# Optimization experiments

Measured on AMD Instinct MI355X. Metric: run time of the kernel, lower is better.

The kernel has to match this reference:

```python
import jax, jax.numpy as jnp
import numpy as np

# Constants matching init_kwargs
N_HEADS = 8
D_MODEL = 256
PATCH_NUM = 128
D_K = D_MODEL // N_HEADS  # 32
TEMP = 0.5
EPS = 1e-10


def setup_inputs() -> dict:
    key = jax.random.key(0)
    ks = jax.random.split(key, 20)
    s = 0.02
    d, h, n = D_MODEL, N_HEADS, PATCH_NUM
    inp = {
        "x": jax.random.normal(ks[0], (32, n, d), dtype=jnp.float32),
        "gumbel_u": jax.random.uniform(ks[1], (h, n, n, 2), dtype=jnp.float32),
        "memory_w": jax.random.normal(ks[2], (n, h * d), dtype=jnp.float32) * s,
        "fc_out_w": jax.random.normal(ks[3], (2 * d, d), dtype=jnp.float32) * s,
        "fc_out_b": jnp.zeros((d,), jnp.float32),
        "fc_cat_w": jax.random.normal(ks[4], (d, 2), dtype=jnp.float32) * s,
        "fc_cat_b": jnp.zeros((2,), jnp.float32),
        "wq": jax.random.normal(ks[5], (d, d), dtype=jnp.float32) * s,
        "bq": jnp.zeros((d,), jnp.float32),
        "wk": jax.random.normal(ks[6], (d, d), dtype=jnp.float32) * s,
        "bk": jnp.zeros((d,), jnp.float32),
        "wv": jax.random.normal(ks[7], (d, d), dtype=jnp.float32) * s,
        "bv": jnp.zeros((d,), jnp.float32),
        "out_w": jax.random.normal(ks[8], (d, d), dtype=jnp.float32) * s,
        "out_b": jnp.zeros((d,), jnp.float32),
        "mlp_w1": jax.random.normal(ks[9], (d, d), dtype=jnp.float32) * s,
        "mlp_b1": jnp.zeros((d,), jnp.float32),
        "mlp_w2": jax.random.normal(ks[10], (d, d), dtype=jnp.float32) * s,
        "mlp_b2": jnp.zeros((d,), jnp.float32),
    }
    return inp


def _forward(x, memory_w, fc_out_w, fc_out_b, fc_cat_w, fc_cat_b,
             wq, bq, wk, bk, wv, bv, out_w, out_b,
             mlp_w1, mlp_b1, mlp_w2, mlp_b2, gumbel_u):
    H, N, D = N_HEADS, PATCH_NUM, D_MODEL
    B = x.shape[0]

    # ---- SSConnectionLearning on memory feats ----
    # memory: Embedding(N, d_model*n_heads) -> feats [H, N, D]
    feats = memory_w.reshape(N, H, D).transpose(1, 0, 2)
    # rel_rec gathers row index i (receiver), rel_send gathers col index j (sender)
    senders = jnp.broadcast_to(feats[:, None, :, :], (H, N, N, D))   # feats[j]
    receivers = jnp.broadcast_to(feats[:, :, None, :], (H, N, N, D))  # feats[i]
    pair = jnp.concatenate([senders, receivers], axis=-1)  # [H,N,N,2D]
    hdn = jax.nn.relu(jnp.einsum('hijc,cd->hijd', pair, fc_out_w) + fc_out_b)
    logits = jnp.einsum('hijd,dk->hijk', hdn, fc_cat_w) + fc_cat_b  # [H,N,N,2]

    # gumbel-softmax, hard=True, straight-through
    g = -jnp.log(-jnp.log(gumbel_u + EPS) + EPS)
    y_soft = jax.nn.softmax((logits + g) / TEMP, axis=-1)
    y_hard = jax.nn.one_hot(jnp.argmax(y_soft, axis=-1), 2, dtype=y_soft.dtype)
    y = jax.lax.stop_gradient(y_hard - y_soft) + y_soft
    conn = y[..., 1]  # [H,N,N] learned sparse connection mask

    # ---- PatchIntegration (GELU MLP, dropout = identity in eval) ----
    xm = jax.nn.gelu(x @ mlp_w1 + mlp_b1)
    xm = xm @ mlp_w2 + mlp_b2

    # ---- Multihead attention masked by connection matrix ----
    q = (xm @ wq + bq).reshape(B, N, H, D_K).transpose(0, 2, 1, 3)  # [B,H,N,dk]
    k = (xm @ wk + bk).reshape(B, N, H, D_K).transpose(0, 2, 1, 3)
    v = (xm @ wv + bv).reshape(B, N, H, D_K).transpose(0, 2, 1, 3)
    scale = D_K ** -0.5
    scores = jnp.einsum('bhqd,bhkd->bhqk', q, k) * scale
    # additive mask: blocked where conn==0 (large negative keeps softmax finite)
    scores = scores + (conn[None] - 1.0) * 1e9
    attn = jax.nn.softmax(scores, axis=-1)
    out = jnp.einsum('bhqk,bhkd->bhqd', attn, v)
    out = out.transpose(0, 2, 1, 3).reshape(B, N, H * D_K)
    out = out @ out_w + out_b
    return out


def reference(x, gumbel_u, memory_w, fc_out_w, fc_out_b, fc_cat_w, fc_cat_b,
              wq, bq, wk, bk, wv, bv, out_w, out_b,
              mlp_w1, mlp_b1, mlp_w2, mlp_b2):
    return _forward(x, memory_w, fc_out_w, fc_out_b, fc_cat_w, fc_cat_b,
                    wq, bq, wk, bk, wv, bv, out_w, out_b,
                    mlp_w1, mlp_b1, mlp_w2, mlp_b2, gumbel_u)
```

## Files before the change

### kernel.cpp

```cpp
#include <hip/hip_runtime.h>
#include <hip/hip_bf16.h>
#include <math.h>


typedef short short8 __attribute__((ext_vector_type(8)));
typedef float f32x4 __attribute__((ext_vector_type(4)));

union V8 { uint4 u; short8 s; };

__device__ __forceinline__ float gelu_f(float x) {
    float inner = 0.7978845608028654f * (x + 0.044715f * x * x * x);
    return 0.5f * x * (1.0f + tanhf(inner));
}
__device__ __forceinline__ void split_bf16(float x, ushort& h, ushort& l) {
    __hip_bfloat16 bh = __float2bfloat16(x);
    float hf = __bfloat162float(bh);
    __hip_bfloat16 bl = __float2bfloat16(x - hf);
    h = __builtin_bit_cast(ushort, bh);
    l = __builtin_bit_cast(ushort, bl);
}
__device__ __forceinline__ ushort bf16bits(float x) {
    return __builtin_bit_cast(ushort, __float2bfloat16(x));
}
__device__ __forceinline__ float bits_to_f(ushort v) {
    return __builtin_bit_cast(float, ((uint)v) << 16);
}
__device__ __forceinline__ short8 lds_frag(const ushort* p) {
    V8 v; v.u = *(const uint4*)p; return v.s;
}


__global__ __launch_bounds__(512) void k_wprep(
    const float* __restrict__ mlp_w1, const float* __restrict__ mlp_w2,
    const float* __restrict__ wq, const float* __restrict__ wk,
    const float* __restrict__ wv, const float* __restrict__ out_w,
    const float* __restrict__ fc_out_w,
    ushort* __restrict__ hi, ushort* __restrict__ lo) {
    __shared__ __align__(16) float xs2[2][32 * 132];
    int bx = blockIdx.x, t = threadIdx.x;
    int half = t >> 8, tl = t & 255;
    int job = bx * 2 + half;
    int m = job >> 4, ks = (job >> 1) & 7, nh = job & 1;
    const float* W = m == 0 ? mlp_w1 : m == 1 ? mlp_w2 : m == 2 ? wq :
                     m == 3 ? wk : m == 4 ? wv : m == 5 ? out_w :
                     m == 6 ? fc_out_w : fc_out_w + 65536;
    ushort* Hm = hi + m * 65536;
    ushort* Lm = lo + m * 65536;
    float* xs = xs2[half];
    #pragma unroll
    for (int p = 0; p < 4; ++p) {
        int idx = p * 256 + tl;
        int row = idx >> 5, c4 = (idx & 31) * 4;
        *(float4*)(xs + row * 132 + c4) =
            *(const float4*)(W + (ks * 32 + row) * 256 + nh * 128 + c4);
    }
    __syncthreads();
    int lane = tl & 63, lr = lane & 15, quad = lane >> 4;
    #pragma unroll
    for (int it = 0; it < 2; ++it) {
        int tgl = (tl >> 6) + 4 * it;
        int tg = nh * 8 + tgl;
        int nl = tgl * 16 + lr;
        ushort hb[8], lb[8];
        #pragma unroll
        for (int j = 0; j < 8; ++j)
            split_bf16(xs[(quad * 8 + j) * 132 + nl], hb[j], lb[j]);
        uint4 ph = { (uint)hb[0] | ((uint)hb[1] << 16), (uint)hb[2] | ((uint)hb[3] << 16),
                     (uint)hb[4] | ((uint)hb[5] << 16), (uint)hb[6] | ((uint)hb[7] << 16) };
        uint4 pl = { (uint)lb[0] | ((uint)lb[1] << 16), (uint)lb[2] | ((uint)lb[3] << 16),
                     (uint)lb[4] | ((uint)lb[5] << 16), (uint)lb[6] | ((uint)lb[7] << 16) };
        int idx = ((tg * 8 + ks) * 64 + lane) * 8;
        *(uint4*)(Hm + idx) = ph;
        *(uint4*)(Lm + idx) = pl;
    }
}

__global__ __launch_bounds__(512) void k_p2(
    const float* __restrict__ memory_w, const float* __restrict__ X,
    const ushort* __restrict__ Whi, const ushort* __restrict__ Wlo,
    const float* __restrict__ b1, const float* __restrict__ b2,
    const float* __restrict__ Bq, const float* __restrict__ Bk,
    const float* __restrict__ Bv,
    float* __restrict__ A, float* __restrict__ Bm,
    ushort* __restrict__ Q, ushort* __restrict__ K, ushort* __restrict__ V) {
    __shared__ __align__(16) union {
        struct { ushort xhi[16 * 264], xlo[16 * 264]; } f;
        struct {
            ushort aHi[16 * 264], aLo[16 * 264];
            ushort bHi[16 * 264], bLo[16 * 264];
        } g;
    } sm;
    int bx = blockIdx.x, t = threadIdx.x;
    if (bx < 64) {
        int rt = bx;
        #pragma unroll
        for (int ii = 0; ii < 2; ++ii) {
            int f4 = ii * 512 + t;
            int rr = f4 >> 6, c = (f4 & 63) * 4;
            int r = rt * 16 + rr;
            int h = r >> 7, n = r & 127;
            float4 xv = *(const float4*)(memory_w + n * 2048 + h * 256 + c);
            ushort hh[4], ll[4];
            split_bf16(xv.x, hh[0], ll[0]); split_bf16(xv.y, hh[1], ll[1]);
            split_bf16(xv.z, hh[2], ll[2]); split_bf16(xv.w, hh[3], ll[3]);
            uint2 ph = { (uint)hh[0] | ((uint)hh[1] << 16), (uint)hh[2] | ((uint)hh[3] << 16) };
            uint2 pl = { (uint)ll[0] | ((uint)ll[1] << 16), (uint)ll[2] | ((uint)ll[3] << 16) };
            *(uint2*)(sm.f.xhi + rr * 264 + c) = ph;
            *(uint2*)(sm.f.xlo + rr * 264 + c) = pl;
        }
        __syncthreads();
        int lane = t & 63, w = t >> 6;
        int lr = lane & 15, quad = lane >> 4;
        int msel = w & 1, cq = w >> 1;
        const uint4* H4 = (const uint4*)(Whi + (6 + msel) * 65536);
        const uint4* L4 = (const uint4*)(Wlo + (6 + msel) * 65536);
        const ushort* ah = sm.f.xhi + lr * 264 + quad * 8;
        const ushort* al = sm.f.xlo + lr * 264 + quad * 8;
        float* O = msel ? Bm : A;
        #pragma unroll
        for (int i = 0; i < 4; ++i) {
            int tg = cq * 4 + i;
            f32x4 acc = {};
            #pragma unroll
            for (int ks = 0; ks < 8; ++ks) {
                short8 a_h = lds_frag(ah + ks * 32);
                short8 a_l = lds_frag(al + ks * 32);
                int off = (tg * 8 + ks) * 64 + lane;
                V8 bh, bl; bh.u = H4[off]; bl.u = L4[off];
                acc = __builtin_amdgcn_mfma_f32_16x16x32_bf16(a_h, bh.s, acc, 0, 0, 0);
                acc = __builtin_amdgcn_mfma_f32_16x16x32_bf16(a_l, bh.s, acc, 0, 0, 0);
                acc = __builtin_amdgcn_mfma_f32_16x16x32_bf16(a_h, bl.s, acc, 0, 0, 0);
            }
            int n0 = tg * 16 + lr;
            #pragma unroll
            for (int r = 0; r < 4; ++r)
                O[(rt * 16 + quad * 4 + r) * 256 + n0] = acc[r];
        }
        return;
    }
    int r0 = (bx - 64) * 16;
    #pragma unroll
    for (int ii = 0; ii < 2; ++ii) {
        int f4 = ii * 512 + t;
        int row = f4 >> 6, c = (f4 & 63) * 4;
        float4 xv = *(const float4*)(X + (r0 + row) * 256 + c);
        ushort h[4], l[4];
        split_bf16(xv.x, h[0], l[0]); split_bf16(xv.y, h[1], l[1]);
        split_bf16(xv.z, h[2], l[2]); split_bf16(xv.w, h[3], l[3]);
        uint2 ph = { (uint)h[0] | ((uint)h[1] << 16), (uint)h[2] | ((uint)h[3] << 16) };
        uint2 pl = { (uint)l[0] | ((uint)l[1] << 16), (uint)l[2] | ((uint)l[3] << 16) };
        *(uint2*)(sm.g.aHi + row * 264 + c) = ph;
        *(uint2*)(sm.g.aLo + row * 264 + c) = pl;
    }
    __syncthreads();
    int lane = t & 63, w = t >> 6;
    int lr = lane & 15, quad = lane >> 4;
    int aoff = lr * 264 + quad * 8;
    {
        const uint4* H4 = (const uint4*)(Whi + 0 * 65536);
        const uint4* L4 = (const uint4*)(Wlo + 0 * 65536);
        f32x4 acc[2] = {};
        #pragma unroll
        for (int ks = 0; ks < 8; ++ks) {
            short8 a_h = lds_frag(sm.g.aHi + aoff + ks * 32);
            short8 a_l = lds_frag(sm.g.aLo + aoff + ks * 32);
            #pragma unroll
            for (int ti = 0; ti < 2; ++ti) {
                int off = ((w * 2 + ti) * 8 + ks) * 64 + lane;
                V8 bh, bl; bh.u = H4[off]; bl.u = L4[off];
                acc[ti] = __builtin_amdgcn_mfma_f32_16x16x32_bf16(a_h, bh.s, acc[ti], 0, 0, 0);
                acc[ti] = __builtin_amdgcn_mfma_f32_16x16x32_bf16(a_l, bh.s, acc[ti], 0, 0, 0);
                acc[ti] = __builtin_amdgcn_mfma_f32_16x16x32_bf16(a_h, bl.s, acc[ti], 0, 0, 0);
            }
        }
        #pragma unroll
        for (int ti = 0; ti < 2; ++ti) {
            int n0 = (w * 2 + ti) * 16 + lr;
            float bb = b1[n0];
            #pragma unroll
            for (int r = 0; r < 4; ++r) {
                float o = gelu_f(acc[ti][r] + bb);
                ushort hh, ll; split_bf16(o, hh, ll);
                int ad = (quad * 4 + r) * 264 + n0;
                sm.g.bHi[ad] = hh; sm.g.bLo[ad] = ll;
            }
        }
    }
    __syncthreads();
    {
        const uint4* H4 = (const uint4*)(Whi + 1 * 65536);
        const uint4* L4 = (const uint4*)(Wlo + 1 * 65536);
        f32x4 acc[2] = {};
        #pragma unroll
        for (int ks = 0; ks < 8; ++ks) {
            short8 a_h = lds_frag(sm.g.bHi + aoff + ks * 32);
            short8 a_l = lds_frag(sm.g.bLo + aoff + ks * 32);
            #pragma unroll
            for (int ti = 0; ti < 2; ++ti) {
                int off = ((w * 2 + ti) * 8 + ks) * 64 + lane;
                V8 bh, bl; bh.u = H4[off]; bl.u = L4[off];
                acc[ti] = __builtin_amdgcn_mfma_f32_16x16x32_bf16(a_h, bh.s, acc[ti], 0, 0, 0);
                acc[ti] = __builtin_amdgcn_mfma_f32_16x16x32_bf16(a_l, bh.s, acc[ti], 0, 0, 0);
                acc[ti] = __builtin_amdgcn_mfma_f32_16x16x32_bf16(a_h, bl.s, acc[ti], 0, 0, 0);
            }
        }
        __syncthreads();
        #pragma unroll
        for (int ti = 0; ti < 2; ++ti) {
            int n0 = (w * 2 + ti) * 16 + lr;
            float bb = b2[n0];
            #pragma unroll
            for (int r = 0; r < 4; ++r) {
                float o = acc[ti][r] + bb;
                ushort hh, ll; split_bf16(o, hh, ll);
                int ad = (quad * 4 + r) * 264 + n0;
                sm.g.aHi[ad] = hh; sm.g.aLo[ad] = ll;
            }
        }
    }
    __syncthreads();
    {
        const uint4* Hq = (const uint4*)(Whi + 2 * 65536);
        const uint4* Lq = (const uint4*)(Wlo + 2 * 65536);
        const uint4* Hk = (const uint4*)(Whi + 3 * 65536);
        const uint4* Lk = (const uint4*)(Wlo + 3 * 65536);
        const uint4* Hv = (const uint4*)(Whi + 4 * 65536);
        const uint4* Lv = (const uint4*)(Wlo + 4 * 65536);
        f32x4 aq[2] = {}, ak[2] = {}, av[2] = {};
        #pragma unroll 2
        for (int ks = 0; ks < 8; ++ks) {
            short8 a_h = lds_frag(sm.g.aHi + aoff + ks * 32);
            short8 a_l = lds_frag(sm.g.aLo + aoff + ks * 32);
            #pragma unroll
            for (int ti = 0; ti < 2; ++ti) {
                int off = ((w * 2 + ti) * 8 + ks) * 64 + lane;
                V8 qh, ql, kh, kl, vh, vl;
                qh.u = Hq[off]; ql.u = Lq[off];
                kh.u = Hk[off]; kl.u = Lk[off];
                vh.u = Hv[off]; vl.u = Lv[off];
                aq[ti] = __builtin_amdgcn_mfma_f32_16x16x32_bf16(a_h, qh.s, aq[ti], 0, 0, 0);
                aq[ti] = __builtin_amdgcn_mfma_f32_16x16x32_bf16(a_l, qh.s, aq[ti], 0, 0, 0);
                aq[ti] = __builtin_amdgcn_mfma_f32_16x16x32_bf16(a_h, ql.s, aq[ti], 0, 0, 0);
                ak[ti] = __builtin_amdgcn_mfma_f32_16x16x32_bf16(a_h, kh.s, ak[ti], 0, 0, 0);
                ak[ti] = __builtin_amdgcn_mfma_f32_16x16x32_bf16(a_l, kh.s, ak[ti], 0, 0, 0);
                ak[ti] = __builtin_amdgcn_mfma_f32_16x16x32_bf16(a_h, kl.s, ak[ti], 0, 0, 0);
                av[ti] = __builtin_amdgcn_mfma_f32_16x16x32_bf16(a_h, vh.s, av[ti], 0, 0, 0);
                av[ti] = __builtin_amdgcn_mfma_f32_16x16x32_bf16(a_l, vh.s, av[ti], 0, 0, 0);
                av[ti] = __builtin_amdgcn_mfma_f32_16x16x32_bf16(a_h, vl.s, av[ti], 0, 0, 0);
            }
        }
        #pragma unroll
        for (int ti = 0; ti < 2; ++ti) {
            int n0 = (w * 2 + ti) * 16 + lr;
            float bq = Bq[n0], bk = Bk[n0], bv = Bv[n0];
            #pragma unroll
            for (int r = 0; r < 4; ++r) {
                int go = (r0 + quad * 4 + r) * 256 + n0;
                Q[go] = bf16bits(aq[ti][r] + bq);
                K[go] = bf16bits(ak[ti][r] + bk);
                V[go] = bf16bits(av[ti][r] + bv);
            }
        }
    }
}

__global__ __launch_bounds__(512) void k_conn(
    const float* __restrict__ A, const float* __restrict__ Bmat,
    const float* __restrict__ fc_out_b, const float* __restrict__ fc_cat_w,
    const float* __restrict__ fc_cat_b, const float* __restrict__ gumbel_u,
    ushort* __restrict__ maskb) {
    __shared__ __align__(16) float sA[16 * 260], sB[32 * 260];
    int bx = blockIdx.x, t = threadIdx.x;
    int h = bx >> 5;
    int rem = bx & 31;
    int it = rem >> 3, jt = rem & 7;
    int i0 = it * 32, j0 = jt * 16;
    int jl = t & 15, il = t >> 4;
    #pragma unroll
    for (int p = 0; p < 6; ++p) {
        int id2 = p * 512 + t;
        if (id2 < 1024) {
            int rr = id2 >> 6, c = (id2 & 63) * 4;
            *(float4*)(sA + rr * 260 + c) =
                *(const float4*)(A + (h * 128 + j0 + rr) * 256 + c);
        } else {
            int id3 = id2 - 1024;
            int rr = id3 >> 6, c = (id3 & 63) * 4;
            float4 bv = *(const float4*)(Bmat + (h * 128 + i0 + rr) * 256 + c);
            float4 fb = *(const float4*)(fc_out_b + c);
            bv.x += fb.x; bv.y += fb.y; bv.z += fb.z; bv.w += fb.w;
            *(float4*)(sB + rr * 260 + c) = bv;
        }
    }
    __syncthreads();
    const float* Ar = sA + jl * 260;
    const float* Br = sB + il * 260;
    float l0 = fc_cat_b[0], l1 = fc_cat_b[1];
    #pragma unroll 4
    for (int d4 = 0; d4 < 64; ++d4) {
        int d = d4 * 4;
        float4 av = *(const float4*)(Ar + d);
        float4 bv = *(const float4*)(Br + d);
        float4 cwA = *(const float4*)(fc_cat_w + d * 2);
        float4 cwB = *(const float4*)(fc_cat_w + d * 2 + 4);
        float h0 = fmaxf(av.x + bv.x, 0.f);
        float h1 = fmaxf(av.y + bv.y, 0.f);
        float h2 = fmaxf(av.z + bv.z, 0.f);
        float h3 = fmaxf(av.w + bv.w, 0.f);
        l0 += h0 * cwA.x + h1 * cwA.z + h2 * cwB.x + h3 * cwB.z;
        l1 += h0 * cwA.y + h1 * cwA.w + h2 * cwB.y + h3 * cwB.w;
    }
    int i = i0 + il, j = j0 + jl;
    float2 uu = *(const float2*)(gumbel_u + ((h * 128 + i) * 128 + j) * 2);
    float g0 = -logf(-logf(uu.x + 1e-10f) + 1e-10f);
    float g1 = -logf(-logf(uu.y + 1e-10f) + 1e-10f);
    bool on = (l1 + g1) > (l0 + g0);
    maskb[(h * 128 + i) * 128 + j] = bf16bits(on ? 0.f : -1e9f);
}

__global__ __launch_bounds__(256) void k_attn_mfma(
    const ushort* __restrict__ Q, const ushort* __restrict__ K,
    const ushort* __restrict__ V, const ushort* __restrict__ maskb,
    float* __restrict__ AO) {
    int bx = blockIdx.x;
    int b = bx >> 4, h = (bx >> 1) & 7, rh = bx & 1;
    int t = threadIdx.x;
    int lane = t & 63, w = t >> 6;
    __shared__ __align__(16) ushort vT[32 * 136];
    __shared__ __align__(16) ushort ps[64 * 136];
    #pragma unroll
    for (int it = 0; it < 2; ++it) {
        int idx = it * 256 + t;
        int key = idx >> 2, dq8 = (idx & 3) * 8;
        V8 vv; vv.u = *(const uint4*)(V + (b * 128 + key) * 256 + h * 32 + dq8);
        #pragma unroll
        for (int m = 0; m < 8; ++m)
            vT[(dq8 + m) * 136 + key] = (ushort)vv.s[m];
    }
    __syncthreads();
    int lr = lane & 15, quad = lane >> 4;
    int rt = rh * 4 + w;
    V8 af;
    af.u = *(const uint4*)(Q + (b * 128 + rt * 16 + lr) * 256 + h * 32 + quad * 8);
    f32x4 s[8];
    #pragma unroll
    for (int ct = 0; ct < 8; ++ct) {
        V8 bf_;
        bf_.u = *(const uint4*)(K + (b * 128 + ct * 16 + lr) * 256 + h * 32 + quad * 8);
        f32x4 z = {0.f, 0.f, 0.f, 0.f};
        s[ct] = __builtin_amdgcn_mfma_f32_16x16x32_bf16(af.s, bf_.s, z, 0, 0, 0);
    }
    const float scale = 0.17677669529663687f;
    const ushort* mrow = maskb + h * 16384;
    #pragma unroll
    for (int r = 0; r < 4; ++r) {
        int lrow = w * 16 + quad * 4 + r;
        int grow = rt * 16 + quad * 4 + r;
        float sv[8];
        float mx = -3.0e38f;
        #pragma unroll
        for (int ct = 0; ct < 8; ++ct) {
            float bias = bits_to_f(mrow[grow * 128 + ct * 16 + lr]);
            sv[ct] = s[ct][r] * scale + bias;
            mx = fmaxf(mx, sv[ct]);
        }
        mx = fmaxf(mx, __shfl_xor(mx, 1));
        mx = fmaxf(mx, __shfl_xor(mx, 2));
        mx = fmaxf(mx, __shfl_xor(mx, 4));
        mx = fmaxf(mx, __shfl_xor(mx, 8));
        float sum = 0.f;
        #pragma unroll
        for (int ct = 0; ct < 8; ++ct) {
            sv[ct] = __expf(sv[ct] - mx);
            sum += sv[ct];
        }
        sum += __shfl_xor(sum, 1);
        sum += __shfl_xor(sum, 2);
        sum += __shfl_xor(sum, 4);
        sum += __shfl_xor(sum, 8);
        float iv = 1.f / sum;
        #pragma unroll
        for (int ct = 0; ct < 8; ++ct)
            ps[lrow * 136 + ct * 16 + lr] = bf16bits(sv[ct] * iv);
    }
    f32x4 o0 = {}, o1 = {};
    #pragma unroll
    for (int kk = 0; kk < 4; ++kk) {
        short8 pa = lds_frag(ps + (w * 16 + lr) * 136 + kk * 32 + quad * 8);
        short8 v0 = lds_frag(vT + lr * 136 + kk * 32 + quad * 8);
        short8 v1 = lds_frag(vT + (16 + lr) * 136 + kk * 32 + quad * 8);
        o0 = __builtin_amdgcn_mfma_f32_16x16x32_bf16(pa, v0, o0, 0, 0, 0);
        o1 = __builtin_amdgcn_mfma_f32_16x16x32_bf16(pa, v1, o1, 0, 0, 0);
    }
    #pragma unroll
    for (int r = 0; r < 4; ++r) {
        int grow = rt * 16 + quad * 4 + r;
        float* op = AO + b * 32768 + grow * 256 + h * 32;
        op[lr] = o0[r];
        op[16 + lr] = o1[r];
    }
}

__global__ __launch_bounds__(256) void k_gemm16(
    const float* __restrict__ X, const ushort* __restrict__ Whi,
    const ushort* __restrict__ Wlo, const float* __restrict__ bias,
    float* __restrict__ Y) {
    __shared__ __align__(16) ushort xhi[16 * 264], xlo[16 * 264];
    int t = threadIdx.x;
    int r0 = blockIdx.x * 16;
    #pragma unroll
    for (int ii = 0; ii < 4; ++ii) {
        int f4 = ii * 256 + t;
        int row = f4 >> 6, c = (f4 & 63) * 4;
        float4 xv = *(const float4*)(X + (r0 + row) * 256 + c);
        ushort h[4], l[4];
        split_bf16(xv.x, h[0], l[0]); split_bf16(xv.y, h[1], l[1]);
        split_bf16(xv.z, h[2], l[2]); split_bf16(xv.w, h[3], l[3]);
        uint2 ph = { (uint)h[0] | ((uint)h[1] << 16), (uint)h[2] | ((uint)h[3] << 16) };
        uint2 pl = { (uint)l[0] | ((uint)l[1] << 16), (uint)l[2] | ((uint)l[3] << 16) };
        *(uint2*)(xhi + row * 264 + c) = ph;
        *(uint2*)(xlo + row * 264 + c) = pl;
    }
    __syncthreads();
    int l = t & 63, w = t >> 6;
    int lr = l & 15, quad = l >> 4;
    int tg = blockIdx.y * 4 + w;
    const ushort* ah = xhi + lr * 264 + quad * 8;
    const ushort* al = xlo + lr * 264 + quad * 8;
    const uint4* H4 = (const uint4*)Whi;
    const uint4* L4 = (const uint4*)Wlo;
    f32x4 acc = {};
    #pragma unroll
    for (int ks = 0; ks < 8; ++ks) {
        short8 a_h = lds_frag(ah + ks * 32);
        short8 a_l = lds_frag(al + ks * 32);
        int off = (tg * 8 + ks) * 64 + l;
        V8 bh, bl; bh.u = H4[off]; bl.u = L4[off];
        acc = __builtin_amdgcn_mfma_f32_16x16x32_bf16(a_h, bh.s, acc, 0, 0, 0);
        acc = __builtin_amdgcn_mfma_f32_16x16x32_bf16(a_l, bh.s, acc, 0, 0, 0);
        acc = __builtin_amdgcn_mfma_f32_16x16x32_bf16(a_h, bl.s, acc, 0, 0, 0);
    }
    int n0 = tg * 16 + lr;
    float bs = bias[n0];
    #pragma unroll
    for (int r = 0; r < 4; ++r)
        Y[(r0 + quad * 4 + r) * 256 + n0] = acc[r] + bs;
}

extern "C" void kernel_launch(void* const* d_in, const int* in_sizes, int n_in,
                              void* d_out, int out_size, void* d_ws, size_t ws_size,
                              hipStream_t stream) {
    const float* x        = (const float*)d_in[0];
    const float* gumbel_u = (const float*)d_in[1];
    const float* memory_w = (const float*)d_in[2];
    const float* fc_out_w = (const float*)d_in[3];
    const float* fc_out_b = (const float*)d_in[4];
    const float* fc_cat_w = (const float*)d_in[5];
    const float* fc_cat_b = (const float*)d_in[6];
    const float* wq       = (const float*)d_in[7];
    const float* bq       = (const float*)d_in[8];
    const float* wk       = (const float*)d_in[9];
    const float* bk       = (const float*)d_in[10];
    const float* wv_      = (const float*)d_in[11];
    const float* bv_      = (const float*)d_in[12];
    const float* out_w    = (const float*)d_in[13];
    const float* out_b    = (const float*)d_in[14];
    const float* mlp_w1   = (const float*)d_in[15];
    const float* mlp_b1   = (const float*)d_in[16];
    const float* mlp_w2   = (const float*)d_in[17];
    const float* mlp_b2   = (const float*)d_in[18];

    float* ws    = (float*)d_ws;
    float* A     = ws;
    float* Bm    = ws + 262144;
    ushort* mask = (ushort*)(ws + 524288);
    ushort* qb   = (ushort*)(ws + 589824);
    ushort* kb   = (ushort*)(ws + 1114112);
    ushort* vb   = (ushort*)(ws + 1638400);
    float* ao    = ws + 2162688;
    ushort* wf_hi = (ushort*)(ws + 3211264);
    ushort* wf_lo = wf_hi + 8 * 65536;
    float* out   = (float*)d_out;

    k_wprep<<<dim3(64), dim3(512), 0, stream>>>(
        mlp_w1, mlp_w2, wq, wk, wv_, out_w, fc_out_w, wf_hi, wf_lo);
    k_p2<<<dim3(320), dim3(512), 0, stream>>>(
        memory_w, x, wf_hi, wf_lo, mlp_b1, mlp_b2, bq, bk, bv_,
        A, Bm, qb, kb, vb);
    k_conn<<<dim3(256), dim3(512), 0, stream>>>(
        A, Bm, fc_out_b, fc_cat_w, fc_cat_b, gumbel_u, mask);
    k_attn_mfma<<<dim3(512), dim3(256), 0, stream>>>(qb, kb, vb, mask, ao);
    k_gemm16<<<dim3(256, 4), dim3(256), 0, stream>>>(ao, wf_hi + 5 * 65536,
                                                     wf_lo + 5 * 65536, out_b, out);
}
```

Before: 145.2 us.

## Write Q/K in head-major layout and V pre-transposed to drop LDS transpose

The projection kernel now writes Q and K as [B,H,N,dk] and V as [B,H,dk,N] instead of the row-major [B,N,D] layout. The attention kernel then loads Q, K and V fragments straight from global memory, so the shared-memory V transpose and its barrier go away. The cost is scattered 2-byte stores for V in the producer kernel (stride 128 elements), which may be poorly coalesced.

Result: no change. 146.3 us (+0.8%).

```diff
diff --git a/kernel.cpp b/kernel.cpp
--- a/kernel.cpp
+++ b/kernel.cpp
@@ -82,7 +82,7 @@
     const float* __restrict__ Bq, const float* __restrict__ Bk,
     const float* __restrict__ Bv,
     float* __restrict__ A, float* __restrict__ Bm,
-    ushort* __restrict__ Q, ushort* __restrict__ K, ushort* __restrict__ V) {
+    ushort* __restrict__ Qn, ushort* __restrict__ Kn, ushort* __restrict__ Vt) {
     __shared__ __align__(16) union {
         struct { ushort xhi[16 * 264], xlo[16 * 264]; } f;
         struct {
@@ -139,22 +139,21 @@
         return;
     }
     int r0 = (bx - 64) * 16;
+    int lane = t & 63, w = t >> 6, lr = lane & 15, quad = lane >> 4;
     #pragma unroll
     for (int ii = 0; ii < 2; ++ii) {
         int f4 = ii * 512 + t;
         int row = f4 >> 6, c = (f4 & 63) * 4;
         float4 xv = *(const float4*)(X + (r0 + row) * 256 + c);
-        ushort h[4], l[4];
-        split_bf16(xv.x, h[0], l[0]); split_bf16(xv.y, h[1], l[1]);
-        split_bf16(xv.z, h[2], l[2]); split_bf16(xv.w, h[3], l[3]);
-        uint2 ph = { (uint)h[0] | ((uint)h[1] << 16), (uint)h[2] | ((uint)h[3] << 16) };
-        uint2 pl = { (uint)l[0] | ((uint)l[1] << 16), (uint)l[2] | ((uint)l[3] << 16) };
+        ushort h4[4], l4[4];
+        split_bf16(xv.x, h4[0], l4[0]); split_bf16(xv.y, h4[1], l4[1]);
+        split_bf16(xv.z, h4[2], l4[2]); split_bf16(xv.w, h4[3], l4[3]);
+        uint2 ph = { (uint)h4[0] | ((uint)h4[1] << 16), (uint)h4[2] | ((uint)h4[3] << 16) };
+        uint2 pl = { (uint)l4[0] | ((uint)l4[1] << 16), (uint)l4[2] | ((uint)l4[3] << 16) };
         *(uint2*)(sm.g.aHi + row * 264 + c) = ph;
         *(uint2*)(sm.g.aLo + row * 264 + c) = pl;
     }
     __syncthreads();
-    int lane = t & 63, w = t >> 6;
-    int lr = lane & 15, quad = lane >> 4;
     int aoff = lr * 264 + quad * 8;
     {
         const uint4* H4 = (const uint4*)(Whi + 0 * 65536);
@@ -252,13 +251,16 @@
         #pragma unroll
         for (int ti = 0; ti < 2; ++ti) {
             int n0 = (w * 2 + ti) * 16 + lr;
-            float bq = Bq[n0], bk = Bk[n0], bv = Bv[n0];
+            int hh = n0 >> 5, dk = n0 & 31;
+            float vbq = Bq[n0], vbk = Bk[n0], vbv = Bv[n0];
             #pragma unroll
             for (int r = 0; r < 4; ++r) {
-                int go = (r0 + quad * 4 + r) * 256 + n0;
-                Q[go] = bf16bits(aq[ti][r] + bq);
-                K[go] = bf16bits(ak[ti][r] + bk);
-                V[go] = bf16bits(av[ti][r] + bv);
+                int row = r0 + quad * 4 + r;
+                int bb = row >> 7, n = row & 127;
+                int bh_ = bb * 8 + hh;
+                Qn[(bh_ * 128 + n) * 32 + dk] = bf16bits(aq[ti][r] + vbq);
+                Kn[(bh_ * 128 + n) * 32 + dk] = bf16bits(ak[ti][r] + vbk);
+                Vt[(bh_ * 32 + dk) * 128 + n] = bf16bits(av[ti][r] + vbv);
             }
         }
     }
@@ -319,34 +321,23 @@
 }
 
 __global__ __launch_bounds__(256) void k_attn_mfma(
-    const ushort* __restrict__ Q, const ushort* __restrict__ K,
-    const ushort* __restrict__ V, const ushort* __restrict__ maskb,
+    const ushort* __restrict__ Qn, const ushort* __restrict__ Kn,
+    const ushort* __restrict__ Vt, const ushort* __restrict__ maskb,
     float* __restrict__ AO) {
+    __shared__ __align__(16) ushort ps[64 * 136];
     int bx = blockIdx.x;
     int b = bx >> 4, h = (bx >> 1) & 7, rh = bx & 1;
     int t = threadIdx.x;
-    int lane = t & 63, w = t >> 6;
-    __shared__ __align__(16) ushort vT[32 * 136];
-    __shared__ __align__(16) ushort ps[64 * 136];
-    #pragma unroll
-    for (int it = 0; it < 2; ++it) {
-        int idx = it * 256 + t;
-        int key = idx >> 2, dq8 = (idx & 3) * 8;
-        V8 vv; vv.u = *(const uint4*)(V + (b * 128 + key) * 256 + h * 32 + dq8);
-        #pragma unroll
-        for (int m = 0; m < 8; ++m)
-            vT[(dq8 + m) * 136 + key] = (ushort)vv.s[m];
-    }
-    __syncthreads();
-    int lr = lane & 15, quad = lane >> 4;
+    int lane = t & 63, w = t >> 6, lr = lane & 15, quad = lane >> 4;
     int rt = rh * 4 + w;
+    int bh_ = b * 8 + h;
     V8 af;
-    af.u = *(const uint4*)(Q + (b * 128 + rt * 16 + lr) * 256 + h * 32 + quad * 8);
+    af.u = *(const uint4*)(Qn + (bh_ * 128 + rt * 16 + lr) * 32 + quad * 8);
     f32x4 s[8];
     #pragma unroll
     for (int ct = 0; ct < 8; ++ct) {
         V8 bf_;
-        bf_.u = *(const uint4*)(K + (b * 128 + ct * 16 + lr) * 256 + h * 32 + quad * 8);
+        bf_.u = *(const uint4*)(Kn + (bh_ * 128 + ct * 16 + lr) * 32 + quad * 8);
         f32x4 z = {0.f, 0.f, 0.f, 0.f};
         s[ct] = __builtin_amdgcn_mfma_f32_16x16x32_bf16(af.s, bf_.s, z, 0, 0, 0);
     }
@@ -387,10 +378,11 @@
     #pragma unroll
     for (int kk = 0; kk < 4; ++kk) {
         short8 pa = lds_frag(ps + (w * 16 + lr) * 136 + kk * 32 + quad * 8);
-        short8 v0 = lds_frag(vT + lr * 136 + kk * 32 + quad * 8);
-        short8 v1 = lds_frag(vT + (16 + lr) * 136 + kk * 32 + quad * 8);
-        o0 = __builtin_amdgcn_mfma_f32_16x16x32_bf16(pa, v0, o0, 0, 0, 0);
-        o1 = __builtin_amdgcn_mfma_f32_16x16x32_bf16(pa, v1, o1, 0, 0, 0);
+        V8 v0, v1;
+        v0.u = *(const uint4*)(Vt + (bh_ * 32 + lr) * 128 + kk * 32 + quad * 8);
+        v1.u = *(const uint4*)(Vt + (bh_ * 32 + 16 + lr) * 128 + kk * 32 + quad * 8);
+        o0 = __builtin_amdgcn_mfma_f32_16x16x32_bf16(pa, v0.s, o0, 0, 0, 0);
+        o1 = __builtin_amdgcn_mfma_f32_16x16x32_bf16(pa, v1.s, o1, 0, 0, 0);
     }
     #pragma unroll
     for (int r = 0; r < 4; ++r) {
@@ -470,26 +462,26 @@
     const float* mlp_w2   = (const float*)d_in[17];
     const float* mlp_b2   = (const float*)d_in[18];
 
-    float* ws    = (float*)d_ws;
-    float* A     = ws;
-    float* Bm    = ws + 262144;
-    ushort* mask = (ushort*)(ws + 524288);
-    ushort* qb   = (ushort*)(ws + 589824);
-    ushort* kb   = (ushort*)(ws + 1114112);
-    ushort* vb   = (ushort*)(ws + 1638400);
-    float* ao    = ws + 2162688;
+    float* ws     = (float*)d_ws;
+    float* A      = ws;
+    float* Bm     = ws + 262144;
+    ushort* mask  = (ushort*)(ws + 524288);
+    ushort* qn    = (ushort*)(ws + 589824);
+    ushort* kn    = (ushort*)(ws + 1114112);
+    ushort* vt    = (ushort*)(ws + 1638400);
+    float* ao     = ws + 2162688;
     ushort* wf_hi = (ushort*)(ws + 3211264);
     ushort* wf_lo = wf_hi + 8 * 65536;
-    float* out   = (float*)d_out;
+    float* out    = (float*)d_out;
 
     k_wprep<<<dim3(64), dim3(512), 0, stream>>>(
         mlp_w1, mlp_w2, wq, wk, wv_, out_w, fc_out_w, wf_hi, wf_lo);
     k_p2<<<dim3(320), dim3(512), 0, stream>>>(
         memory_w, x, wf_hi, wf_lo, mlp_b1, mlp_b2, bq, bk, bv_,
-        A, Bm, qb, kb, vb);
+        A, Bm, qn, kn, vt);
     k_conn<<<dim3(256), dim3(512), 0, stream>>>(
         A, Bm, fc_out_b, fc_cat_w, fc_cat_b, gumbel_u, mask);
-    k_attn_mfma<<<dim3(512), dim3(256), 0, stream>>>(qb, kb, vb, mask, ao);
+    k_attn_mfma<<<dim3(512), dim3(256), 0, stream>>>(qn, kn, vt, mask, ao);
     k_gemm16<<<dim3(256, 4), dim3(256), 0, stream>>>(ao, wf_hi + 5 * 65536,
                                                      wf_lo + 5 * 65536, out_b, out);
 }
```
